# Kernel optimization log

Measured on AMD Instinct MI355X. Metric: run time of the kernel, lower is better.

Reference implementation:

```python
import jax, jax.numpy as jnp
import numpy as np

N_USERS = 50000
N_ENTITIES = 100000
N_NODES = N_USERS + N_ENTITIES
N_EDGES = 3000000
EMB_DIM = 64
WEIGHT_SIZES = [64, 64, 32, 16]  # [emb_dim] + weight_size
BATCH = 8192
LEAKY_SLOPE = 0.2  # KGAT (TF reference) uses leaky_relu alpha=0.2
EPS = 1e-12


def setup_inputs() -> dict:
    key = jax.random.key(0)
    ks = jax.random.split(key, 24)
    inp = {}
    inp["users"] = jax.random.randint(ks[0], (BATCH,), 0, N_USERS, dtype=jnp.int32)
    inp["pos_items"] = jax.random.randint(ks[1], (BATCH,), 0, N_ENTITIES, dtype=jnp.int32)
    inp["neg_items"] = jax.random.randint(ks[2], (BATCH,), 0, N_ENTITIES, dtype=jnp.int32)
    inp["all_h"] = jax.random.randint(ks[3], (N_EDGES,), 0, N_NODES, dtype=jnp.int32)
    inp["all_t"] = jax.random.randint(ks[4], (N_EDGES,), 0, N_NODES, dtype=jnp.int32)
    inp["A_values"] = jax.random.uniform(ks[5], (N_EDGES,), dtype=jnp.float32)
    inp["user_embed"] = jax.random.normal(ks[6], (N_USERS, EMB_DIM), dtype=jnp.float32) * 0.1
    inp["entity_embed"] = jax.random.normal(ks[7], (N_ENTITIES, EMB_DIM), dtype=jnp.float32) * 0.1
    ki = 8
    for k in range(3):
        din, dout = WEIGHT_SIZES[k], WEIGHT_SIZES[k + 1]
        scale = float(np.sqrt(2.0 / (din + dout)))  # xavier-ish
        inp[f"W_gc_{k}"] = jax.random.normal(ks[ki], (din, dout), dtype=jnp.float32) * scale; ki += 1
        inp[f"b_gc_{k}"] = jax.random.normal(ks[ki], (1, dout), dtype=jnp.float32) * scale; ki += 1
        inp[f"W_bi_{k}"] = jax.random.normal(ks[ki], (din, dout), dtype=jnp.float32) * scale; ki += 1
        inp[f"b_bi_{k}"] = jax.random.normal(ks[ki], (1, dout), dtype=jnp.float32) * scale; ki += 1
    return inp


def _bi_interaction(ego, all_h, all_t, A_values, layers, n_nodes):
    # KGAT bi-interaction aggregator over edge-list sparse adjacency.
    outs = [ego]
    for (W_gc, b_gc, W_bi, b_bi) in layers:
        # sparse A @ ego : gather tails, weight by attention, scatter-add to heads
        msgs = A_values[:, None] * ego[all_t]                       # [E, d]
        side = jax.ops.segment_sum(msgs, all_h, num_segments=n_nodes)  # [N, d]
        sum_emb = jax.nn.leaky_relu((ego + side) @ W_gc + b_gc, negative_slope=LEAKY_SLOPE)
        bi_emb = jax.nn.leaky_relu((ego * side) @ W_bi + b_bi, negative_slope=LEAKY_SLOPE)
        ego = sum_emb + bi_emb
        norm = ego / jnp.maximum(jnp.linalg.norm(ego, axis=1, keepdims=True), EPS)
        outs.append(norm)
    return jnp.concatenate(outs, axis=1)  # [N, 64+64+32+16]


def reference(users, pos_items, neg_items, all_h, all_t, A_values,
              user_embed, entity_embed,
              W_gc_0, b_gc_0, W_bi_0, b_bi_0,
              W_gc_1, b_gc_1, W_bi_1, b_bi_1,
              W_gc_2, b_gc_2, W_bi_2, b_bi_2):
    n_users = user_embed.shape[0]
    n_nodes = n_users + entity_embed.shape[0]
    ego = jnp.concatenate([user_embed, entity_embed], axis=0)  # [N, 64]
    layers = [(W_gc_0, b_gc_0, W_bi_0, b_bi_0),
              (W_gc_1, b_gc_1, W_bi_1, b_bi_1),
              (W_gc_2, b_gc_2, W_bi_2, b_bi_2)]
    all_emb = _bi_interaction(ego, all_h, all_t, A_values, layers, n_nodes)
    ua, ea = all_emb[:n_users], all_emb[n_users:]
    u_e = ua[users]
    pos_i_e = ea[pos_items]
    neg_i_e = ea[neg_items]
    return (u_e, pos_i_e, neg_i_e)
```

## Files before the change

### kernel.cpp

```cpp
#include <hip/hip_runtime.h>
#include <math.h>

#define N_USERS    50000
#define N_ENTITIES 100000
#define N_NODES    150000
#define N_EDGES    3000000
#define BATCH      8192
#define SLOPE      0.2f
#define EPSF       1e-12f

#define NBUK   2344
#define CAP    1536
#define BLK_E  12288
#define NPB    ((N_EDGES + BLK_E - 1) / BLK_E)
#define PBLK   1024
#define EPT    (BLK_E / PBLK)
#define CH     4096
#define GC_STRIDE 16

__device__ __forceinline__ unsigned f2bf(float f) {
    unsigned u = __float_as_uint(f);
    return (u + 0x7FFFu + ((u >> 16) & 1u)) >> 16;
}
__device__ __forceinline__ float bf_lo(unsigned d) { return __uint_as_float(d << 16); }
__device__ __forceinline__ float bf_hi(unsigned d) { return __uint_as_float(d & 0xFFFF0000u); }

__global__ __launch_bounds__(256)
void cast0_k(const float* __restrict__ user_emb, const float* __restrict__ ent_emb,
             unsigned short* __restrict__ ego0_bf) {
    int idx = blockIdx.x * 256 + threadIdx.x;
    const int total = N_NODES * 64 / 4;
    if (idx >= total) return;
    int ge = idx * 4;
    const float* src = (ge < N_USERS * 64) ? user_emb + ge
                                           : ent_emb + (ge - N_USERS * 64);
    float4 v = *(const float4*)src;
    ushort4 o;
    o.x = (unsigned short)f2bf(v.x);
    o.y = (unsigned short)f2bf(v.y);
    o.z = (unsigned short)f2bf(v.z);
    o.w = (unsigned short)f2bf(v.w);
    *(ushort4*)(ego0_bf + ge) = o;
}

__global__ __launch_bounds__(PBLK)
void partition_k(const int* __restrict__ all_h, const int* __restrict__ all_t,
                 const float* __restrict__ A,
                 int* __restrict__ gcursor, int2* __restrict__ rec) {
    __shared__ int pos[NBUK];
    __shared__ int gofs[NBUK];
    __shared__ int wsum[PBLK / 64];
    __shared__ int2 srec[CH];
    __shared__ int  sdst[CH];

    int t = threadIdx.x;
    for (int i = t; i < NBUK; i += PBLK) pos[i] = 0;
    __syncthreads();

    int e0 = blockIdx.x * BLK_E;
    int e1 = e0 + BLK_E; if (e1 > N_EDGES) e1 = N_EDGES;
    int tot = e1 - e0;

    int h[EPT]; int tt[EPT]; float aa[EPT];
    #pragma unroll
    for (int k = 0; k < EPT; ++k) {
        int e = e0 + k * PBLK + t;
        bool v = e < e1;
        h[k]  = v ? all_h[e] : -1;
        tt[k] = v ? all_t[e] : 0;
        aa[k] = v ? A[e] : 0.f;
    }
    #pragma unroll
    for (int k = 0; k < EPT; ++k)
        if (h[k] >= 0) atomicAdd(&pos[h[k] >> 6], 1);
    __syncthreads();

    int c[3], g[3];
    int i0 = t * 3;
    int tsum = 0;
    #pragma unroll
    for (int j = 0; j < 3; ++j) {
        int idx = i0 + j;
        c[j] = (idx < NBUK) ? pos[idx] : 0;
        tsum += c[j];
        g[j] = (idx < NBUK && c[j]) ? atomicAdd(&gcursor[idx * GC_STRIDE], c[j]) : 0;
    }

    int lane = t & 63, w = t >> 6;
    int incl = tsum;
    #pragma unroll
    for (int off = 1; off < 64; off <<= 1) {
        int x = __shfl_up(incl, off, 64);
        if (lane >= off) incl += x;
    }
    if (lane == 63) wsum[w] = incl;
    __syncthreads();
    int wbase = 0;
    for (int j = 0; j < w; ++j) wbase += wsum[j];
    int excl = wbase + (incl - tsum);

    #pragma unroll
    for (int j = 0; j < 3; ++j) {
        int idx = i0 + j;
        if (idx < NBUK) { pos[idx] = excl; gofs[idx] = g[j] - excl; }
        excl += c[j];
    }
    __syncthreads();

    int pp[EPT], gd[EPT];
    #pragma unroll
    for (int k = 0; k < EPT; ++k) {
        if (h[k] >= 0) {
            int b = h[k] >> 6;
            int p = atomicAdd(&pos[b], 1);
            pp[k] = p;
            int gr = gofs[b] + p;
            gd[k] = (gr < CAP) ? b * CAP + gr : -1;
        } else {
            pp[k] = -1; gd[k] = -1;
        }
    }

    for (int base = 0; base < tot; base += CH) {
        __syncthreads();
        int lim = tot - base; if (lim > CH) lim = CH;
        #pragma unroll
        for (int k = 0; k < EPT; ++k) {
            int s = pp[k] - base;
            if (s >= 0 && s < CH) {
                srec[s] = make_int2(tt[k] | ((h[k] & 63) << 18), __float_as_int(aa[k]));
                sdst[s] = gd[k];
            }
        }
        __syncthreads();
        for (int s = t; s < lim; s += PBLK) {
            int d = sdst[s];
            if (d >= 0) rec[d] = srec[s];
        }
    }
}

__global__ __launch_bounds__(256)
void local_sort_k(const int* __restrict__ gcursor, int2* __restrict__ rec,
                  int2* __restrict__ range) {
    __shared__ int2 sin[CAP];
    __shared__ int2 sout[CAP];
    __shared__ int cnt64[64];
    __shared__ int pos64[64];
    int b = blockIdx.x, t = threadIdx.x;
    int cnt = gcursor[(size_t)b * GC_STRIDE]; if (cnt > CAP) cnt = CAP;

    if (t < 64) cnt64[t] = 0;
    __syncthreads();

    for (int i = t; i < cnt; i += 256) {
        int2 p = rec[(size_t)b * CAP + i];
        sin[i] = p;
        atomicAdd(&cnt64[(p.x >> 18) & 63], 1);
    }
    __syncthreads();

    if (t < 64) {
        int v = cnt64[t];
        int sum = v;
        #pragma unroll
        for (int off = 1; off < 64; off <<= 1) {
            int x = __shfl_up(sum, off, 64);
            if (t >= off) sum += x;
        }
        pos64[t] = sum - v;
    }
    __syncthreads();

    for (int i = t; i < cnt; i += 256) {
        int2 p = sin[i];
        int l = (p.x >> 18) & 63;
        int dst = atomicAdd(&pos64[l], 1);
        sout[dst] = make_int2(p.x & 0x3FFFF, p.y);
    }
    __syncthreads();

    for (int i = t; i < cnt; i += 256)
        rec[(size_t)b * CAP + i] = sout[i];

    if (t < 64) {
        int v = cnt64[t];
        int sum = v;
        #pragma unroll
        for (int off = 1; off < 64; off <<= 1) {
            int x = __shfl_up(sum, off, 64);
            if (t >= off) sum += x;
        }
        int start = b * CAP + (sum - v);
        int node = b * 64 + t;
        if (node < N_NODES) range[node] = make_int2(start, start + v);
    }
}

template<int DIN>
__global__ __launch_bounds__(256)
void side_k(const int2* __restrict__ range, const int2* __restrict__ rec,
            const unsigned short* __restrict__ tab, float* __restrict__ side) {
    constexpr int LPR = DIN / 8;
    constexpr int EPW = 64 / LPR;

    int w = threadIdx.x >> 6;
    int lane = threadIdx.x & 63;
    int h = blockIdx.x * 4 + w;

    int2 rg = range[h];
    int e0 = rg.x, e1 = rg.y;
    int g = lane / LPR;
    int q = lane % LPR;

    float acc[8];
    #pragma unroll
    for (int j = 0; j < 8; ++j) acc[j] = 0.f;

    for (int e = e0; e < e1; e += 2 * EPW) {
        int i0 = e + g;
        int i1 = e + EPW + g;
        int c0 = i0 < e1 ? i0 : e1 - 1;
        int c1 = i1 < e1 ? i1 : e1 - 1;
        int2 p0 = rec[c0];
        int2 p1 = rec[c1];
        float a0 = (i0 < e1) ? __int_as_float(p0.y) : 0.f;
        float a1 = (i1 < e1) ? __int_as_float(p1.y) : 0.f;
        uint4 d0 = *(const uint4*)(tab + (size_t)p0.x * DIN + q * 8);
        uint4 d1 = *(const uint4*)(tab + (size_t)p1.x * DIN + q * 8);
        acc[0] = fmaf(a0, bf_lo(d0.x), acc[0]);
        acc[1] = fmaf(a0, bf_hi(d0.x), acc[1]);
        acc[2] = fmaf(a0, bf_lo(d0.y), acc[2]);
        acc[3] = fmaf(a0, bf_hi(d0.y), acc[3]);
        acc[4] = fmaf(a0, bf_lo(d0.z), acc[4]);
        acc[5] = fmaf(a0, bf_hi(d0.z), acc[5]);
        acc[6] = fmaf(a0, bf_lo(d0.w), acc[6]);
        acc[7] = fmaf(a0, bf_hi(d0.w), acc[7]);
        acc[0] = fmaf(a1, bf_lo(d1.x), acc[0]);
        acc[1] = fmaf(a1, bf_hi(d1.x), acc[1]);
        acc[2] = fmaf(a1, bf_lo(d1.y), acc[2]);
        acc[3] = fmaf(a1, bf_hi(d1.y), acc[3]);
        acc[4] = fmaf(a1, bf_lo(d1.z), acc[4]);
        acc[5] = fmaf(a1, bf_hi(d1.z), acc[5]);
        acc[6] = fmaf(a1, bf_lo(d1.w), acc[6]);
        acc[7] = fmaf(a1, bf_hi(d1.w), acc[7]);
    }

    #pragma unroll
    for (int off = LPR; off < 64; off <<= 1)
        #pragma unroll
        for (int j = 0; j < 8; ++j) acc[j] += __shfl_xor(acc[j], off, 64);

    if (lane < LPR) {
        float* dst = side + (size_t)h * DIN + q * 8;
        *(float4*)dst       = make_float4(acc[0], acc[1], acc[2], acc[3]);
        *(float4*)(dst + 4) = make_float4(acc[4], acc[5], acc[6], acc[7]);
    }
}

template<int DIN, int DOUT, int TILE_ROWS, bool CONCAT, bool OUT_BF>
__global__ __launch_bounds__(256)
void transform_k(const unsigned short* __restrict__ ego_in,
                 const float* __restrict__ user_emb, const float* __restrict__ ent_emb,
                 const float* __restrict__ side,
                 const float* __restrict__ Wgc, const float* __restrict__ bgc,
                 const float* __restrict__ Wbi, const float* __restrict__ bbi,
                 void* __restrict__ ego_out) {
    constexpr int NG = DOUT / 8;
    constexpr int RG = 256 / NG;
    constexpr int RT = TILE_ROWS / RG;
    constexpr int STRIDE = DIN + 4;
    constexpr int KC8 = DIN / 8;

    __shared__ float sWgc[DIN * DOUT], sWbi[DIN * DOUT];
    __shared__ float sU[TILE_ROWS * STRIDE], sV[TILE_ROWS * STRIDE];

    int t = threadIdx.x;

    for (int i = t * 4; i < DIN * DOUT; i += 1024) {
        *(float4*)&sWgc[i] = *(const float4*)&Wgc[i];
        *(float4*)&sWbi[i] = *(const float4*)&Wbi[i];
    }

    int base = blockIdx.x * TILE_ROWS;
    for (int f = t; f < TILE_ROWS * KC8; f += 256) {
        int row = f / KC8, c8 = f % KC8;
        int n = base + row;
        int nc = n < N_NODES ? n : N_NODES - 1;
        float ev[8];
        if (CONCAT) {
            const float* erow = (nc < N_USERS) ? user_emb + (size_t)nc * 64
                                               : ent_emb + (size_t)(nc - N_USERS) * 64;
            float4 a = *(const float4*)(erow + c8 * 8);
            float4 b = *(const float4*)(erow + c8 * 8 + 4);
            ev[0] = a.x; ev[1] = a.y; ev[2] = a.z; ev[3] = a.w;
            ev[4] = b.x; ev[5] = b.y; ev[6] = b.z; ev[7] = b.w;
        } else {
            uint4 d = *(const uint4*)(ego_in + (size_t)nc * DIN + c8 * 8);
            ev[0] = bf_lo(d.x); ev[1] = bf_hi(d.x);
            ev[2] = bf_lo(d.y); ev[3] = bf_hi(d.y);
            ev[4] = bf_lo(d.z); ev[5] = bf_hi(d.z);
            ev[6] = bf_lo(d.w); ev[7] = bf_hi(d.w);
        }
        const float* srow = side + (size_t)nc * DIN + c8 * 8;
        float4 s0 = *(const float4*)srow;
        float4 s1 = *(const float4*)(srow + 4);
        float sv8[8] = {s0.x, s0.y, s0.z, s0.w, s1.x, s1.y, s1.z, s1.w};
        float* pu = &sU[row * STRIDE + c8 * 8];
        float* pv = &sV[row * STRIDE + c8 * 8];
        *(float4*)pu       = make_float4(ev[0] + sv8[0], ev[1] + sv8[1], ev[2] + sv8[2], ev[3] + sv8[3]);
        *(float4*)(pu + 4) = make_float4(ev[4] + sv8[4], ev[5] + sv8[5], ev[6] + sv8[6], ev[7] + sv8[7]);
        *(float4*)pv       = make_float4(ev[0] * sv8[0], ev[1] * sv8[1], ev[2] * sv8[2], ev[3] * sv8[3]);
        *(float4*)(pv + 4) = make_float4(ev[4] * sv8[4], ev[5] * sv8[5], ev[6] * sv8[6], ev[7] * sv8[7]);
    }
    __syncthreads();

    int cg = t % NG, rgi = t / NG;
    int c0 = cg * 8;
    int r0 = rgi * RT;

    float accg[RT][8], accb[RT][8];
    #pragma unroll
    for (int r = 0; r < RT; ++r)
        #pragma unroll
        for (int j = 0; j < 8; ++j) { accg[r][j] = 0.f; accb[r][j] = 0.f; }

    for (int k = 0; k < DIN; k += 4) {
        float4 u4[RT], v4[RT];
        #pragma unroll
        for (int r = 0; r < RT; ++r) {
            u4[r] = *(const float4*)&sU[(r0 + r) * STRIDE + k];
            v4[r] = *(const float4*)&sV[(r0 + r) * STRIDE + k];
        }
        #pragma unroll
        for (int kk = 0; kk < 4; ++kk) {
            float4 wg0 = *(const float4*)&sWgc[(k + kk) * DOUT + c0];
            float4 wg1 = *(const float4*)&sWgc[(k + kk) * DOUT + c0 + 4];
            float4 wb0 = *(const float4*)&sWbi[(k + kk) * DOUT + c0];
            float4 wb1 = *(const float4*)&sWbi[(k + kk) * DOUT + c0 + 4];
            #pragma unroll
            for (int r = 0; r < RT; ++r) {
                float u = ((const float*)&u4[r])[kk];
                float v = ((const float*)&v4[r])[kk];
                accg[r][0] = fmaf(u, wg0.x, accg[r][0]);
                accg[r][1] = fmaf(u, wg0.y, accg[r][1]);
                accg[r][2] = fmaf(u, wg0.z, accg[r][2]);
                accg[r][3] = fmaf(u, wg0.w, accg[r][3]);
                accg[r][4] = fmaf(u, wg1.x, accg[r][4]);
                accg[r][5] = fmaf(u, wg1.y, accg[r][5]);
                accg[r][6] = fmaf(u, wg1.z, accg[r][6]);
                accg[r][7] = fmaf(u, wg1.w, accg[r][7]);
                accb[r][0] = fmaf(v, wb0.x, accb[r][0]);
                accb[r][1] = fmaf(v, wb0.y, accb[r][1]);
                accb[r][2] = fmaf(v, wb0.z, accb[r][2]);
                accb[r][3] = fmaf(v, wb0.w, accb[r][3]);
                accb[r][4] = fmaf(v, wb1.x, accb[r][4]);
                accb[r][5] = fmaf(v, wb1.y, accb[r][5]);
                accb[r][6] = fmaf(v, wb1.z, accb[r][6]);
                accb[r][7] = fmaf(v, wb1.w, accb[r][7]);
            }
        }
    }

    float4 bg0 = *(const float4*)&bgc[c0];
    float4 bg1 = *(const float4*)&bgc[c0 + 4];
    float4 bb0 = *(const float4*)&bbi[c0];
    float4 bb1 = *(const float4*)&bbi[c0 + 4];
    float bg[8] = {bg0.x, bg0.y, bg0.z, bg0.w, bg1.x, bg1.y, bg1.z, bg1.w};
    float bb[8] = {bb0.x, bb0.y, bb0.z, bb0.w, bb1.x, bb1.y, bb1.z, bb1.w};

    #pragma unroll
    for (int r = 0; r < RT; ++r) {
        int n = base + r0 + r;
        if (n < N_NODES) {
            float o[8];
            #pragma unroll
            for (int j = 0; j < 8; ++j) {
                float gg = accg[r][j] + bg[j];
                float b2 = accb[r][j] + bb[j];
                gg = gg > 0.f ? gg : SLOPE * gg;
                b2 = b2 > 0.f ? b2 : SLOPE * b2;
                o[j] = gg + b2;
            }
            if (OUT_BF) {
                unsigned short* dst = (unsigned short*)ego_out + (size_t)n * DOUT + c0;
                uint4 wv;
                wv.x = f2bf(o[0]) | (f2bf(o[1]) << 16);
                wv.y = f2bf(o[2]) | (f2bf(o[3]) << 16);
                wv.z = f2bf(o[4]) | (f2bf(o[5]) << 16);
                wv.w = f2bf(o[6]) | (f2bf(o[7]) << 16);
                *(uint4*)dst = wv;
            } else {
                float* dst = (float*)ego_out + (size_t)n * DOUT + c0;
                *(float4*)dst       = make_float4(o[0], o[1], o[2], o[3]);
                *(float4*)(dst + 4) = make_float4(o[4], o[5], o[6], o[7]);
            }
        }
    }
}

__global__ __launch_bounds__(64)
void gather_k(const int* __restrict__ users, const int* __restrict__ pos,
              const int* __restrict__ neg,
              const float* __restrict__ user_emb, const float* __restrict__ ent_emb,
              const unsigned short* __restrict__ ego1_bf,
              const unsigned short* __restrict__ ego2_bf,
              const float* __restrict__ ego3,
              float* __restrict__ out) {
    int r = blockIdx.x;
    int lane = threadIdx.x;
    int which = r / BATCH;
    int i = r - which * BATCH;
    int node;
    if (which == 0)      node = users[i];
    else if (which == 1) node = N_USERS + pos[i];
    else                 node = N_USERS + neg[i];

    float* o = out + (size_t)r * 176;

    float x0 = (node < N_USERS) ? user_emb[(size_t)node * 64 + lane]
                                : ent_emb[(size_t)(node - N_USERS) * 64 + lane];
    o[lane] = x0;

    float x1 = __uint_as_float((unsigned)ego1_bf[(size_t)node * 64 + lane] << 16);
    float ss = x1 * x1;
    #pragma unroll
    for (int off = 32; off > 0; off >>= 1) ss += __shfl_xor(ss, off, 64);
    o[64 + lane] = x1 / fmaxf(sqrtf(ss), EPSF);

    float x2 = (lane < 32)
        ? __uint_as_float((unsigned)ego2_bf[(size_t)node * 32 + lane] << 16) : 0.f;
    float ss2 = x2 * x2;
    #pragma unroll
    for (int off = 32; off > 0; off >>= 1) ss2 += __shfl_xor(ss2, off, 64);
    if (lane < 32) o[128 + lane] = x2 / fmaxf(sqrtf(ss2), EPSF);

    float x3 = (lane < 16) ? ego3[(size_t)node * 16 + lane] : 0.f;
    float ss3 = x3 * x3;
    #pragma unroll
    for (int off = 32; off > 0; off >>= 1) ss3 += __shfl_xor(ss3, off, 64);
    if (lane < 16) o[160 + lane] = x3 / fmaxf(sqrtf(ss3), EPSF);
}

extern "C" void kernel_launch(void* const* d_in, const int* in_sizes, int n_in,
                              void* d_out, int out_size, void* d_ws, size_t ws_size,
                              hipStream_t stream) {
    const int*   users    = (const int*)d_in[0];
    const int*   pos      = (const int*)d_in[1];
    const int*   neg      = (const int*)d_in[2];
    const int*   all_h    = (const int*)d_in[3];
    const int*   all_t    = (const int*)d_in[4];
    const float* A        = (const float*)d_in[5];
    const float* user_emb = (const float*)d_in[6];
    const float* ent_emb  = (const float*)d_in[7];
    const float* Wgc0 = (const float*)d_in[8];
    const float* bgc0 = (const float*)d_in[9];
    const float* Wbi0 = (const float*)d_in[10];
    const float* bbi0 = (const float*)d_in[11];
    const float* Wgc1 = (const float*)d_in[12];
    const float* bgc1 = (const float*)d_in[13];
    const float* Wbi1 = (const float*)d_in[14];
    const float* bbi1 = (const float*)d_in[15];
    const float* Wgc2 = (const float*)d_in[16];
    const float* bgc2 = (const float*)d_in[17];
    const float* Wbi2 = (const float*)d_in[18];
    const float* bbi2 = (const float*)d_in[19];

    char* p = (char*)d_ws;
    int*   gcursor = (int*)p;            p += ((size_t)NBUK * GC_STRIDE * 4 + 255) & ~255ull;
    int2*  rec     = (int2*)p;           char* rec_base = p;
    p += ((size_t)NBUK * CAP * 8 + 255) & ~255ull;
    int2*  range   = (int2*)p;           p += ((size_t)N_NODES * 8 + 255) & ~255ull;
    float* side    = (float*)p;          p += ((size_t)N_NODES * 64 * 4 + 255) & ~255ull;
    unsigned short* ego0_bf = (unsigned short*)p; p += ((size_t)N_NODES * 64 * 2 + 255) & ~255ull;
    unsigned short* ego1_bf = (unsigned short*)p; p += ((size_t)N_NODES * 64 * 2 + 255) & ~255ull;
    unsigned short* ego2_bf = (unsigned short*)p; p += ((size_t)N_NODES * 32 * 2 + 255) & ~255ull;
    float* ego3    = (float*)rec_base;
    float* out     = (float*)d_out;

    const int nodeBlocks = N_NODES / 4;

    (void)hipMemsetAsync(gcursor, 0, (size_t)NBUK * GC_STRIDE * 4, stream);
    cast0_k<<<(N_NODES * 64 / 4 + 255) / 256, 256, 0, stream>>>(user_emb, ent_emb, ego0_bf);
    partition_k<<<NPB, PBLK, 0, stream>>>(all_h, all_t, A, gcursor, rec);
    local_sort_k<<<NBUK, 256, 0, stream>>>(gcursor, rec, range);

    side_k<64><<<nodeBlocks, 256, 0, stream>>>(range, rec, ego0_bf, side);
    transform_k<64, 64, 64, true, true><<<(N_NODES + 63) / 64, 256, 0, stream>>>(
        nullptr, user_emb, ent_emb, side, Wgc0, bgc0, Wbi0, bbi0, ego1_bf);

    side_k<64><<<nodeBlocks, 256, 0, stream>>>(range, rec, ego1_bf, side);
    transform_k<64, 32, 64, false, true><<<(N_NODES + 63) / 64, 256, 0, stream>>>(
        ego1_bf, nullptr, nullptr, side, Wgc1, bgc1, Wbi1, bbi1, ego2_bf);

    side_k<32><<<nodeBlocks, 256, 0, stream>>>(range, rec, ego2_bf, side);
    transform_k<32, 16, 128, false, false><<<(N_NODES + 127) / 128, 256, 0, stream>>>(
        ego2_bf, nullptr, nullptr, side, Wgc2, bgc2, Wbi2, bbi2, ego3);

    gather_k<<<3 * BATCH, 64, 0, stream>>>(
        users, pos, neg, user_emb, ent_emb, ego1_bf, ego2_bf, ego3, out);
}
```

Baseline: 484.5 us.

## Fuse sparse aggregation with dense transform into one kernel per layer

Merges the side_k gather/aggregate kernel and the transform_k matmul into a single fused_k kernel per layer. Each 1024-thread block aggregates neighbor messages for 64 nodes directly into shared memory, then runs the small dense transform, so the fp32 side buffer is never written to or read back from global memory. Launches drop from six to three. In exchange the transform loses register tiling: each thread now handles one row and a few columns with scalar LDS weight reads. Large blocks plus the 8-block launch bound may also limit occupancy or add register pressure.

```diff
diff --git a/kernel.cpp b/kernel.cpp
--- a/kernel.cpp
+++ b/kernel.cpp
@@ -197,204 +197,155 @@
     }
 }
 
-template<int DIN>
-__global__ __launch_bounds__(256)
-void side_k(const int2* __restrict__ range, const int2* __restrict__ rec,
-            const unsigned short* __restrict__ tab, float* __restrict__ side) {
+template<int DIN, int DOUT, bool CONCAT, bool OUT_BF>
+__global__ __launch_bounds__(1024, 8)
+void fused_k(const int2* __restrict__ range, const int2* __restrict__ rec,
+             const unsigned short* __restrict__ tab,
+             const float* __restrict__ user_emb, const float* __restrict__ ent_emb,
+             const float* __restrict__ Wgc, const float* __restrict__ bgc,
+             const float* __restrict__ Wbi, const float* __restrict__ bbi,
+             void* __restrict__ ego_out) {
     constexpr int LPR = DIN / 8;
     constexpr int EPW = 64 / LPR;
-
-    int w = threadIdx.x >> 6;
-    int lane = threadIdx.x & 63;
-    int h = blockIdx.x * 4 + w;
-
-    int2 rg = range[h];
-    int e0 = rg.x, e1 = rg.y;
-    int g = lane / LPR;
-    int q = lane % LPR;
-
-    float acc[8];
-    #pragma unroll
-    for (int j = 0; j < 8; ++j) acc[j] = 0.f;
-
-    for (int e = e0; e < e1; e += 2 * EPW) {
-        int i0 = e + g;
-        int i1 = e + EPW + g;
-        int c0 = i0 < e1 ? i0 : e1 - 1;
-        int c1 = i1 < e1 ? i1 : e1 - 1;
-        int2 p0 = rec[c0];
-        int2 p1 = rec[c1];
-        float a0 = (i0 < e1) ? __int_as_float(p0.y) : 0.f;
-        float a1 = (i1 < e1) ? __int_as_float(p1.y) : 0.f;
-        uint4 d0 = *(const uint4*)(tab + (size_t)p0.x * DIN + q * 8);
-        uint4 d1 = *(const uint4*)(tab + (size_t)p1.x * DIN + q * 8);
-        acc[0] = fmaf(a0, bf_lo(d0.x), acc[0]);
-        acc[1] = fmaf(a0, bf_hi(d0.x), acc[1]);
-        acc[2] = fmaf(a0, bf_lo(d0.y), acc[2]);
-        acc[3] = fmaf(a0, bf_hi(d0.y), acc[3]);
-        acc[4] = fmaf(a0, bf_lo(d0.z), acc[4]);
-        acc[5] = fmaf(a0, bf_hi(d0.z), acc[5]);
-        acc[6] = fmaf(a0, bf_lo(d0.w), acc[6]);
-        acc[7] = fmaf(a0, bf_hi(d0.w), acc[7]);
-        acc[0] = fmaf(a1, bf_lo(d1.x), acc[0]);
-        acc[1] = fmaf(a1, bf_hi(d1.x), acc[1]);
-        acc[2] = fmaf(a1, bf_lo(d1.y), acc[2]);
-        acc[3] = fmaf(a1, bf_hi(d1.y), acc[3]);
-        acc[4] = fmaf(a1, bf_lo(d1.z), acc[4]);
-        acc[5] = fmaf(a1, bf_hi(d1.z), acc[5]);
-        acc[6] = fmaf(a1, bf_lo(d1.w), acc[6]);
-        acc[7] = fmaf(a1, bf_hi(d1.w), acc[7]);
-    }
-
-    #pragma unroll
-    for (int off = LPR; off < 64; off <<= 1)
-        #pragma unroll
-        for (int j = 0; j < 8; ++j) acc[j] += __shfl_xor(acc[j], off, 64);
-
-    if (lane < LPR) {
-        float* dst = side + (size_t)h * DIN + q * 8;
-        *(float4*)dst       = make_float4(acc[0], acc[1], acc[2], acc[3]);
-        *(float4*)(dst + 4) = make_float4(acc[4], acc[5], acc[6], acc[7]);
-    }
-}
-
-template<int DIN, int DOUT, int TILE_ROWS, bool CONCAT, bool OUT_BF>
-__global__ __launch_bounds__(256)
-void transform_k(const unsigned short* __restrict__ ego_in,
-                 const float* __restrict__ user_emb, const float* __restrict__ ent_emb,
-                 const float* __restrict__ side,
-                 const float* __restrict__ Wgc, const float* __restrict__ bgc,
-                 const float* __restrict__ Wbi, const float* __restrict__ bbi,
-                 void* __restrict__ ego_out) {
-    constexpr int NG = DOUT / 8;
-    constexpr int RG = 256 / NG;
-    constexpr int RT = TILE_ROWS / RG;
     constexpr int STRIDE = DIN + 4;
-    constexpr int KC8 = DIN / 8;
+    constexpr int C = DOUT / 16;
 
     __shared__ float sWgc[DIN * DOUT], sWbi[DIN * DOUT];
-    __shared__ float sU[TILE_ROWS * STRIDE], sV[TILE_ROWS * STRIDE];
+    __shared__ float sU[64 * STRIDE], sV[64 * STRIDE];
 
     int t = threadIdx.x;
 
-    for (int i = t * 4; i < DIN * DOUT; i += 1024) {
+    for (int i = t * 4; i < DIN * DOUT; i += 4096) {
         *(float4*)&sWgc[i] = *(const float4*)&Wgc[i];
         *(float4*)&sWbi[i] = *(const float4*)&Wbi[i];
     }
 
-    int base = blockIdx.x * TILE_ROWS;
-    for (int f = t; f < TILE_ROWS * KC8; f += 256) {
-        int row = f / KC8, c8 = f % KC8;
-        int n = base + row;
-        int nc = n < N_NODES ? n : N_NODES - 1;
-        float ev[8];
-        if (CONCAT) {
-            const float* erow = (nc < N_USERS) ? user_emb + (size_t)nc * 64
-                                               : ent_emb + (size_t)(nc - N_USERS) * 64;
-            float4 a = *(const float4*)(erow + c8 * 8);
-            float4 b = *(const float4*)(erow + c8 * 8 + 4);
-            ev[0] = a.x; ev[1] = a.y; ev[2] = a.z; ev[3] = a.w;
-            ev[4] = b.x; ev[5] = b.y; ev[6] = b.z; ev[7] = b.w;
-        } else {
-            uint4 d = *(const uint4*)(ego_in + (size_t)nc * DIN + c8 * 8);
-            ev[0] = bf_lo(d.x); ev[1] = bf_hi(d.x);
-            ev[2] = bf_lo(d.y); ev[3] = bf_hi(d.y);
-            ev[4] = bf_lo(d.z); ev[5] = bf_hi(d.z);
-            ev[6] = bf_lo(d.w); ev[7] = bf_hi(d.w);
-        }
-        const float* srow = side + (size_t)nc * DIN + c8 * 8;
-        float4 s0 = *(const float4*)srow;
-        float4 s1 = *(const float4*)(srow + 4);
-        float sv8[8] = {s0.x, s0.y, s0.z, s0.w, s1.x, s1.y, s1.z, s1.w};
-        float* pu = &sU[row * STRIDE + c8 * 8];
-        float* pv = &sV[row * STRIDE + c8 * 8];
-        *(float4*)pu       = make_float4(ev[0] + sv8[0], ev[1] + sv8[1], ev[2] + sv8[2], ev[3] + sv8[3]);
-        *(float4*)(pu + 4) = make_float4(ev[4] + sv8[4], ev[5] + sv8[5], ev[6] + sv8[6], ev[7] + sv8[7]);
-        *(float4*)pv       = make_float4(ev[0] * sv8[0], ev[1] * sv8[1], ev[2] * sv8[2], ev[3] * sv8[3]);
-        *(float4*)(pv + 4) = make_float4(ev[4] * sv8[4], ev[5] * sv8[5], ev[6] * sv8[6], ev[7] * sv8[7]);
-    }
-    __syncthreads();
-
-    int cg = t % NG, rgi = t / NG;
-    int c0 = cg * 8;
-    int r0 = rgi * RT;
-
-    float accg[RT][8], accb[RT][8];
-    #pragma unroll
-    for (int r = 0; r < RT; ++r)
-        #pragma unroll
-        for (int j = 0; j < 8; ++j) { accg[r][j] = 0.f; accb[r][j] = 0.f; }
+    int w = t >> 6, lane = t & 63;
+    int nb = blockIdx.x * 64;
+    int g = lane / LPR, q = lane % LPR;
+
+    for (int j = 0; j < 4; ++j) {
+        int node = nb + w * 4 + j;
+        if (node >= N_NODES) break;
+
+        int2 rg = range[node];
+        int e0 = rg.x, e1 = rg.y;
+
+        float acc[8];
+        #pragma unroll
+        for (int i = 0; i < 8; ++i) acc[i] = 0.f;
+
+        for (int e = e0; e < e1; e += 2 * EPW) {
+            int i0 = e + g;
+            int i1 = e + EPW + g;
+            int c0e = i0 < e1 ? i0 : e1 - 1;
+            int c1e = i1 < e1 ? i1 : e1 - 1;
+            int2 p0 = rec[c0e];
+            int2 p1 = rec[c1e];
+            float a0 = (i0 < e1) ? __int_as_float(p0.y) : 0.f;
+            float a1 = (i1 < e1) ? __int_as_float(p1.y) : 0.f;
+            uint4 d0 = *(const uint4*)(tab + (unsigned)(p0.x * DIN) + q * 8);
+            uint4 d1 = *(const uint4*)(tab + (unsigned)(p1.x * DIN) + q * 8);
+            acc[0] = fmaf(a0, bf_lo(d0.x), acc[0]);
+            acc[1] = fmaf(a0, bf_hi(d0.x), acc[1]);
+            acc[2] = fmaf(a0, bf_lo(d0.y), acc[2]);
+            acc[3] = fmaf(a0, bf_hi(d0.y), acc[3]);
+            acc[4] = fmaf(a0, bf_lo(d0.z), acc[4]);
+            acc[5] = fmaf(a0, bf_hi(d0.z), acc[5]);
+            acc[6] = fmaf(a0, bf_lo(d0.w), acc[6]);
+            acc[7] = fmaf(a0, bf_hi(d0.w), acc[7]);
+            acc[0] = fmaf(a1, bf_lo(d1.x), acc[0]);
+            acc[1] = fmaf(a1, bf_hi(d1.x), acc[1]);
+            acc[2] = fmaf(a1, bf_lo(d1.y), acc[2]);
+            acc[3] = fmaf(a1, bf_hi(d1.y), acc[3]);
+            acc[4] = fmaf(a1, bf_lo(d1.z), acc[4]);
+            acc[5] = fmaf(a1, bf_hi(d1.z), acc[5]);
+            acc[6] = fmaf(a1, bf_lo(d1.w), acc[6]);
+            acc[7] = fmaf(a1, bf_hi(d1.w), acc[7]);
+        }
+
+        #pragma unroll
+        for (int off = LPR; off < 64; off <<= 1)
+            #pragma unroll
+            for (int i = 0; i < 8; ++i) acc[i] += __shfl_xor(acc[i], off, 64);
+
+        if (lane < LPR) {
+            float ev[8];
+            if (CONCAT) {
+                const float* erow = (node < N_USERS)
+                    ? user_emb + (size_t)node * 64
+                    : ent_emb + (size_t)(node - N_USERS) * 64;
+                float4 a = *(const float4*)(erow + q * 8);
+                float4 b = *(const float4*)(erow + q * 8 + 4);
+                ev[0] = a.x; ev[1] = a.y; ev[2] = a.z; ev[3] = a.w;
+                ev[4] = b.x; ev[5] = b.y; ev[6] = b.z; ev[7] = b.w;
+            } else {
+                uint4 d = *(const uint4*)(tab + (unsigned)(node * DIN) + q * 8);
+                ev[0] = bf_lo(d.x); ev[1] = bf_hi(d.x);
+                ev[2] = bf_lo(d.y); ev[3] = bf_hi(d.y);
+                ev[4] = bf_lo(d.z); ev[5] = bf_hi(d.z);
+                ev[6] = bf_lo(d.w); ev[7] = bf_hi(d.w);
+            }
+            int row = w * 4 + j;
+            float* pu = &sU[row * STRIDE + q * 8];
+            float* pv = &sV[row * STRIDE + q * 8];
+            *(float4*)pu       = make_float4(ev[0] + acc[0], ev[1] + acc[1], ev[2] + acc[2], ev[3] + acc[3]);
+            *(float4*)(pu + 4) = make_float4(ev[4] + acc[4], ev[5] + acc[5], ev[6] + acc[6], ev[7] + acc[7]);
+            *(float4*)pv       = make_float4(ev[0] * acc[0], ev[1] * acc[1], ev[2] * acc[2], ev[3] * acc[3]);
+            *(float4*)(pv + 4) = make_float4(ev[4] * acc[4], ev[5] * acc[5], ev[6] * acc[6], ev[7] * acc[7]);
+        }
+    }
+    __syncthreads();
+
+    int cg = t & 15, row = t >> 4;
+    int c0 = cg * C;
+
+    float accg[C], accb[C];
+    #pragma unroll
+    for (int c = 0; c < C; ++c) { accg[c] = 0.f; accb[c] = 0.f; }
 
     for (int k = 0; k < DIN; k += 4) {
-        float4 u4[RT], v4[RT];
-        #pragma unroll
-        for (int r = 0; r < RT; ++r) {
-            u4[r] = *(const float4*)&sU[(r0 + r) * STRIDE + k];
-            v4[r] = *(const float4*)&sV[(r0 + r) * STRIDE + k];
-        }
+        float4 u4 = *(const float4*)&sU[row * STRIDE + k];
+        float4 v4 = *(const float4*)&sV[row * STRIDE + k];
         #pragma unroll
         for (int kk = 0; kk < 4; ++kk) {
-            float4 wg0 = *(const float4*)&sWgc[(k + kk) * DOUT + c0];
-            float4 wg1 = *(const float4*)&sWgc[(k + kk) * DOUT + c0 + 4];
-            float4 wb0 = *(const float4*)&sWbi[(k + kk) * DOUT + c0];
-            float4 wb1 = *(const float4*)&sWbi[(k + kk) * DOUT + c0 + 4];
+            float u = ((const float*)&u4)[kk];
+            float v = ((const float*)&v4)[kk];
             #pragma unroll
-            for (int r = 0; r < RT; ++r) {
-                float u = ((const float*)&u4[r])[kk];
-                float v = ((const float*)&v4[r])[kk];
-                accg[r][0] = fmaf(u, wg0.x, accg[r][0]);
-                accg[r][1] = fmaf(u, wg0.y, accg[r][1]);
-                accg[r][2] = fmaf(u, wg0.z, accg[r][2]);
-                accg[r][3] = fmaf(u, wg0.w, accg[r][3]);
-                accg[r][4] = fmaf(u, wg1.x, accg[r][4]);
-                accg[r][5] = fmaf(u, wg1.y, accg[r][5]);
-                accg[r][6] = fmaf(u, wg1.z, accg[r][6]);
-                accg[r][7] = fmaf(u, wg1.w, accg[r][7]);
-                accb[r][0] = fmaf(v, wb0.x, accb[r][0]);
-                accb[r][1] = fmaf(v, wb0.y, accb[r][1]);
-                accb[r][2] = fmaf(v, wb0.z, accb[r][2]);
-                accb[r][3] = fmaf(v, wb0.w, accb[r][3]);
-                accb[r][4] = fmaf(v, wb1.x, accb[r][4]);
-                accb[r][5] = fmaf(v, wb1.y, accb[r][5]);
-                accb[r][6] = fmaf(v, wb1.z, accb[r][6]);
-                accb[r][7] = fmaf(v, wb1.w, accb[r][7]);
+            for (int c = 0; c < C; ++c) {
+                accg[c] = fmaf(u, sWgc[(k + kk) * DOUT + c0 + c], accg[c]);
+                accb[c] = fmaf(v, sWbi[(k + kk) * DOUT + c0 + c], accb[c]);
             }
         }
     }
 
-    float4 bg0 = *(const float4*)&bgc[c0];
-    float4 bg1 = *(const float4*)&bgc[c0 + 4];
-    float4 bb0 = *(const float4*)&bbi[c0];
-    float4 bb1 = *(const float4*)&bbi[c0 + 4];
-    float bg[8] = {bg0.x, bg0.y, bg0.z, bg0.w, bg1.x, bg1.y, bg1.z, bg1.w};
-    float bb[8] = {bb0.x, bb0.y, bb0.z, bb0.w, bb1.x, bb1.y, bb1.z, bb1.w};
-
-    #pragma unroll
-    for (int r = 0; r < RT; ++r) {
-        int n = base + r0 + r;
-        if (n < N_NODES) {
-            float o[8];
-            #pragma unroll
-            for (int j = 0; j < 8; ++j) {
-                float gg = accg[r][j] + bg[j];
-                float b2 = accb[r][j] + bb[j];
-                gg = gg > 0.f ? gg : SLOPE * gg;
-                b2 = b2 > 0.f ? b2 : SLOPE * b2;
-                o[j] = gg + b2;
-            }
-            if (OUT_BF) {
-                unsigned short* dst = (unsigned short*)ego_out + (size_t)n * DOUT + c0;
-                uint4 wv;
+    int n = nb + row;
+    if (n < N_NODES) {
+        float o[C];
+        #pragma unroll
+        for (int c = 0; c < C; ++c) {
+            float gg = accg[c] + bgc[c0 + c];
+            float b2 = accb[c] + bbi[c0 + c];
+            gg = gg > 0.f ? gg : SLOPE * gg;
+            b2 = b2 > 0.f ? b2 : SLOPE * b2;
+            o[c] = gg + b2;
+        }
+        if (OUT_BF) {
+            unsigned short* dst = (unsigned short*)ego_out + (size_t)n * DOUT + c0;
+            if (C == 4) {
+                uint2 wv;
                 wv.x = f2bf(o[0]) | (f2bf(o[1]) << 16);
                 wv.y = f2bf(o[2]) | (f2bf(o[3]) << 16);
-                wv.z = f2bf(o[4]) | (f2bf(o[5]) << 16);
-                wv.w = f2bf(o[6]) | (f2bf(o[7]) << 16);
-                *(uint4*)dst = wv;
+                *(uint2*)dst = wv;
+            } else if (C == 2) {
+                *(unsigned*)dst = f2bf(o[0]) | (f2bf(o[1]) << 16);
             } else {
-                float* dst = (float*)ego_out + (size_t)n * DOUT + c0;
-                *(float4*)dst       = make_float4(o[0], o[1], o[2], o[3]);
-                *(float4*)(dst + 4) = make_float4(o[4], o[5], o[6], o[7]);
+                *dst = (unsigned short)f2bf(o[0]);
             }
+        } else {
+            float* dst = (float*)ego_out + (size_t)n * DOUT + c0;
+            #pragma unroll
+            for (int c = 0; c < C; ++c) dst[c] = o[c];
         }
     }
 }
@@ -471,31 +422,25 @@
     int2*  rec     = (int2*)p;           char* rec_base = p;
     p += ((size_t)NBUK * CAP * 8 + 255) & ~255ull;
     int2*  range   = (int2*)p;           p += ((size_t)N_NODES * 8 + 255) & ~255ull;
-    float* side    = (float*)p;          p += ((size_t)N_NODES * 64 * 4 + 255) & ~255ull;
     unsigned short* ego0_bf = (unsigned short*)p; p += ((size_t)N_NODES * 64 * 2 + 255) & ~255ull;
     unsigned short* ego1_bf = (unsigned short*)p; p += ((size_t)N_NODES * 64 * 2 + 255) & ~255ull;
     unsigned short* ego2_bf = (unsigned short*)p; p += ((size_t)N_NODES * 32 * 2 + 255) & ~255ull;
     float* ego3    = (float*)rec_base;
     float* out     = (float*)d_out;
 
-    const int nodeBlocks = N_NODES / 4;
-
     (void)hipMemsetAsync(gcursor, 0, (size_t)NBUK * GC_STRIDE * 4, stream);
     cast0_k<<<(N_NODES * 64 / 4 + 255) / 256, 256, 0, stream>>>(user_emb, ent_emb, ego0_bf);
     partition_k<<<NPB, PBLK, 0, stream>>>(all_h, all_t, A, gcursor, rec);
     local_sort_k<<<NBUK, 256, 0, stream>>>(gcursor, rec, range);
 
-    side_k<64><<<nodeBlocks, 256, 0, stream>>>(range, rec, ego0_bf, side);
-    transform_k<64, 64, 64, true, true><<<(N_NODES + 63) / 64, 256, 0, stream>>>(
-        nullptr, user_emb, ent_emb, side, Wgc0, bgc0, Wbi0, bbi0, ego1_bf);
-
-    side_k<64><<<nodeBlocks, 256, 0, stream>>>(range, rec, ego1_bf, side);
-    transform_k<64, 32, 64, false, true><<<(N_NODES + 63) / 64, 256, 0, stream>>>(
-        ego1_bf, nullptr, nullptr, side, Wgc1, bgc1, Wbi1, bbi1, ego2_bf);
-
-    side_k<32><<<nodeBlocks, 256, 0, stream>>>(range, rec, ego2_bf, side);
-    transform_k<32, 16, 128, false, false><<<(N_NODES + 127) / 128, 256, 0, stream>>>(
-        ego2_bf, nullptr, nullptr, side, Wgc2, bgc2, Wbi2, bbi2, ego3);
+    fused_k<64, 64, true, true><<<NBUK, 1024, 0, stream>>>(
+        range, rec, ego0_bf, user_emb, ent_emb, Wgc0, bgc0, Wbi0, bbi0, ego1_bf);
+
+    fused_k<64, 32, false, true><<<NBUK, 1024, 0, stream>>>(
+        range, rec, ego1_bf, nullptr, nullptr, Wgc1, bgc1, Wbi1, bbi1, ego2_bf);
+
+    fused_k<32, 16, false, false><<<NBUK, 1024, 0, stream>>>(
+        range, rec, ego2_bf, nullptr, nullptr, Wgc2, bgc2, Wbi2, bbi2, ego3);
 
     gather_k<<<3 * BATCH, 64, 0, stream>>>(
         users, pos, neg, user_emb, ent_emb, ego1_bf, ego2_bf, ego3, out);
```

Result: slower. 545.3 us (+12.5%).
